# Performance work log

Measured on AMD Instinct MI355X. Metric: run time of the kernel, lower is better.

The kernel has to match this reference:

```python
import jax, jax.numpy as jnp
import numpy as np

D_MODEL = 1024
NUM_HEADS = 16
D_HEAD = D_MODEL // NUM_HEADS


def setup_inputs() -> dict:
    key = jax.random.key(0)
    kx, kq, kk, kv, ko = jax.random.split(key, 5)
    b, seq = 4, 2048
    x = jax.random.normal(kx, (b, seq, D_MODEL), dtype=jnp.float32)
    # Original uses ones for q/k/v and randn for output; use small random weights
    # for a numerically meaningful baseline of the same math.
    Wq = jax.random.normal(kq, (D_MODEL, D_MODEL), dtype=jnp.float32) * 0.02
    Wk = jax.random.normal(kk, (D_MODEL, D_MODEL), dtype=jnp.float32) * 0.02
    Wv = jax.random.normal(kv, (D_MODEL, D_MODEL), dtype=jnp.float32) * 0.02
    Wo = jax.random.normal(ko, (D_MODEL, D_MODEL), dtype=jnp.float32) * 0.02
    return {"x": x, "Wq": Wq, "Wk": Wk, "Wv": Wv, "Wo": Wo}


def reference(x, Wq, Wk, Wv, Wo):
    b, seq, d = x.shape
    h, dh = NUM_HEADS, D_HEAD

    def split_heads(t):  # [b, s, d] -> [b, h, s, dh]
        return t.reshape(b, seq, h, dh).transpose(0, 2, 1, 3)

    q = split_heads(x @ Wq.T)
    k = split_heads(x @ Wk.T)
    v = split_heads(x @ Wv.T)

    scores = jnp.einsum('bhqd,bhkd->bhqk', q, k) / jnp.sqrt(jnp.float32(dh))
    causal = jnp.tril(jnp.ones((seq, seq), dtype=bool))
    scores = jnp.where(causal, scores, -jnp.inf)
    attn = jax.nn.softmax(scores, axis=-1)
    out = jnp.einsum('bhqk,bhkd->bhqd', attn, v)  # [b, h, s, dh]
    out = out.transpose(0, 2, 1, 3).reshape(b, seq, d)
    return out @ Wo.T
```

## Files before the change

kernel.cpp:

```cpp
#include <hip/hip_runtime.h>
#include <stdint.h>

typedef unsigned short u16;
typedef __attribute__((ext_vector_type(8))) __bf16 bf16x8;
typedef __attribute__((ext_vector_type(4))) float f32x4;

#define AS1 __attribute__((address_space(1)))
#define AS3 __attribute__((address_space(3)))
#define LOG2E 1.4426950408889634f

#define BAR() __builtin_amdgcn_s_barrier()
#define VMC5() asm volatile("s_waitcnt vmcnt(5)" ::: "memory")
#define VMC0() asm volatile("s_waitcnt vmcnt(0)" ::: "memory")

__device__ __forceinline__ u16 f2bf(float f) {
    union { __bf16 h; u16 u; } cv;
    cv.h = (__bf16)f;
    return cv.u;
}

__device__ __forceinline__ float vmax4(f32x4 x) {
    return fmaxf(fmaxf(x[0], x[1]), fmaxf(x[2], x[3]));
}
__device__ __forceinline__ float vsum4(f32x4 x) {
    return (x[0] + x[1]) + (x[2] + x[3]);
}

__global__ __launch_bounds__(256) void cvt_kernel(
    const float* __restrict__ src, u16* __restrict__ dst, int n8)
{
    int i = blockIdx.x * 256 + threadIdx.x;
    if (i >= n8) return;
    const float4* s = (const float4*)src;
    float4 f0 = s[(size_t)i * 2], f1 = s[(size_t)i * 2 + 1];
    ushort4 a, b;
    a.x = f2bf(f0.x); a.y = f2bf(f0.y); a.z = f2bf(f0.z); a.w = f2bf(f0.w);
    b.x = f2bf(f1.x); b.y = f2bf(f1.y); b.z = f2bf(f1.z); b.w = f2bf(f1.w);
    ((ushort4*)dst)[(size_t)i * 2]     = a;
    ((ushort4*)dst)[(size_t)i * 2 + 1] = b;
}

__global__ __launch_bounds__(256) void cvt3_kernel(
    const float* __restrict__ wq, const float* __restrict__ wk,
    const float* __restrict__ wv, u16* __restrict__ dst)
{
    int i = blockIdx.x * 256 + threadIdx.x;
    int seg = i >> 17;
    const float* s = (seg == 0) ? wq : (seg == 1) ? wk : wv;
    float sc = (seg == 0) ? 0.125f : 1.0f;
    int j = i & 131071;
    const float4* sp = (const float4*)s;
    float4 f0 = sp[(size_t)j * 2], f1 = sp[(size_t)j * 2 + 1];
    ushort4 a, b;
    a.x = f2bf(f0.x * sc); a.y = f2bf(f0.y * sc); a.z = f2bf(f0.z * sc); a.w = f2bf(f0.w * sc);
    b.x = f2bf(f1.x * sc); b.y = f2bf(f1.y * sc); b.z = f2bf(f1.z * sc); b.w = f2bf(f1.w * sc);
    ((ushort4*)dst)[(size_t)i * 2]     = a;
    ((ushort4*)dst)[(size_t)i * 2 + 1] = b;
}

#define QBUF 28672

__device__ __forceinline__ void stage_A(
    const u16* __restrict__ G, int kt, int hm, u16* region, int t)
{
    int w6 = t & ~63;
#pragma unroll
    for (int i = 0; i < 2; ++i) {
        int s = i * 512 + t;
        int r = s >> 3;
        int j = (s & 7) ^ (r & 7);
        int row = (r & 63) + ((r >> 6) << 7) + (hm << 6);
        const u16* g = G + (size_t)row * 1024 + kt * 64 + j * 8;
        u16* lp = region + (i * 512 + w6) * 8;
        __builtin_amdgcn_global_load_lds((AS1 unsigned int*)g, (AS3 unsigned int*)lp, 16, 0, 0);
    }
}

__device__ __forceinline__ void stage_B01(
    const u16* __restrict__ G, int kt, u16* region, int t)
{
    int w6 = t & ~63;
#pragma unroll
    for (int i = 0; i < 2; ++i) {
        int s = i * 512 + t;
        int r = s >> 3;
        int j = (s & 7) ^ (r & 7);
        const u16* g = G + (size_t)r * 1024 + kt * 64 + j * 8;
        u16* lp = region + (i * 512 + w6) * 8;
        __builtin_amdgcn_global_load_lds((AS1 unsigned int*)g, (AS3 unsigned int*)lp, 16, 0, 0);
    }
}

__device__ __forceinline__ void stage_B2(
    const u16* __restrict__ G, int kt, u16* region, int t)
{
    int r = t >> 3;
    int j = (t & 7) ^ (r & 7);
    const u16* g = G + (size_t)(128 + r) * 1024 + kt * 64 + j * 8;
    u16* lp = region + 8192 + ((t & ~63)) * 8;
    __builtin_amdgcn_global_load_lds((AS1 unsigned int*)g, (AS3 unsigned int*)lp, 16, 0, 0);
}

__device__ __forceinline__ bf16x8 fragr(const u16* region, int row, int j) {
    int byte = row * 128 + ((j ^ (row & 7)) << 4);
    return *(const bf16x8*)((const char*)region + byte);
}

__global__ __launch_bounds__(512, 2) void gemm_qkv_256(
    const u16* __restrict__ X, const u16* __restrict__ W3, u16* __restrict__ QKV)
{
    __shared__ __attribute__((aligned(16))) u16 lds[57344];

    const int t  = threadIdx.x;
    const int l  = t & 63, w = t >> 6;
    const int wm = w >> 2, wn = w & 3;
    const int lr = l & 15, lg = l >> 4;

    int bid = (int)blockIdx.x;
    int wg  = (bid & 7) * 64 + (bid >> 3);
    int mx  = wg >> 4, ny = wg & 15;
    const int mb = mx * 256, nb = ny * 192;
    const u16* A = X  + (size_t)mb * 1024;
    const u16* B = W3 + (size_t)nb * 1024;

    const int NT = 16;

    stage_A  (A, 0, 0, lds + 0,             t);
    stage_B01(B, 0,    lds + 16384,         t);
    stage_B2 (B, 0,    lds + 16384,         t);
    stage_A  (A, 0, 1, lds + 8192,          t);
    stage_A  (A, 1, 0, lds + QBUF + 0,      t);
    stage_B01(B, 1,    lds + QBUF + 16384,  t);
    stage_B2 (B, 1,    lds + QBUF + 16384,  t);
    VMC5();
    BAR();

    f32x4 acc[8][3];
#pragma unroll
    for (int i = 0; i < 8; ++i)
#pragma unroll
        for (int j = 0; j < 3; ++j) acc[i][j] = f32x4{0.f, 0.f, 0.f, 0.f};

    const int brow0 = wn * 48;

    for (int kt = 0; kt < NT; ++kt) {
        const int p = kt & 1;
        u16* A0r = lds + p * QBUF;
        u16* A1r = A0r + 8192;
        u16* Br  = A0r + 16384;
        u16* A1n = lds + (p ^ 1) * QBUF + 8192;
        u16* Bn  = lds + p * QBUF + 16384;

        bf16x8 af[4][2], bf[3][2];

#pragma unroll
        for (int mi = 0; mi < 4; ++mi)
#pragma unroll
            for (int ks = 0; ks < 2; ++ks)
                af[mi][ks] = fragr(A0r, wm * 64 + mi * 16 + lr, ks * 4 + lg);
#pragma unroll
        for (int ni = 0; ni < 2; ++ni)
#pragma unroll
            for (int ks = 0; ks < 2; ++ks)
                bf[ni][ks] = fragr(Br, brow0 + ni * 16 + lr, ks * 4 + lg);
        if (kt + 1 < NT) stage_A(A, kt + 1, 1, A1n, t);
        BAR();
        __builtin_amdgcn_s_setprio(1);
#pragma unroll
        for (int mi = 0; mi < 4; ++mi)
#pragma unroll
            for (int ni = 0; ni < 2; ++ni)
#pragma unroll
                for (int ks = 0; ks < 2; ++ks)
                    acc[mi][ni] = __builtin_amdgcn_mfma_f32_16x16x32_bf16(af[mi][ks], bf[ni][ks], acc[mi][ni], 0, 0, 0);
        __builtin_amdgcn_s_setprio(0);
        BAR();

#pragma unroll
        for (int ks = 0; ks < 2; ++ks)
            bf[2][ks] = fragr(Br, brow0 + 32 + lr, ks * 4 + lg);
        if (kt + 2 < NT) stage_A(A, kt + 2, 0, A0r, t);
        BAR();
        __builtin_amdgcn_s_setprio(1);
#pragma unroll
        for (int mi = 0; mi < 4; ++mi)
#pragma unroll
            for (int ks = 0; ks < 2; ++ks)
                acc[mi][2] = __builtin_amdgcn_mfma_f32_16x16x32_bf16(af[mi][ks], bf[2][ks], acc[mi][2], 0, 0, 0);
        __builtin_amdgcn_s_setprio(0);
        BAR();

#pragma unroll
        for (int mi = 0; mi < 4; ++mi)
#pragma unroll
            for (int ks = 0; ks < 2; ++ks)
                af[mi][ks] = fragr(A1r, wm * 64 + mi * 16 + lr, ks * 4 + lg);
        if (kt + 2 < NT) stage_B01(B, kt + 2, Bn, t);
        BAR();
        __builtin_amdgcn_s_setprio(1);
#pragma unroll
        for (int mi = 0; mi < 4; ++mi)
#pragma unroll
            for (int ni = 0; ni < 2; ++ni)
#pragma unroll
                for (int ks = 0; ks < 2; ++ks)
                    acc[4 + mi][ni] = __builtin_amdgcn_mfma_f32_16x16x32_bf16(af[mi][ks], bf[ni][ks], acc[4 + mi][ni], 0, 0, 0);
        __builtin_amdgcn_s_setprio(0);
        BAR();

        if (kt + 2 < NT) {
            stage_B2(B, kt + 2, Bn, t);
            VMC5();
        } else if (kt + 1 < NT) {
            VMC0();
        }
        BAR();
        __builtin_amdgcn_s_setprio(1);
#pragma unroll
        for (int mi = 0; mi < 4; ++mi)
#pragma unroll
            for (int ks = 0; ks < 2; ++ks)
                acc[4 + mi][2] = __builtin_amdgcn_mfma_f32_16x16x32_bf16(af[mi][ks], bf[2][ks], acc[4 + mi][2], 0, 0, 0);
        __builtin_amdgcn_s_setprio(0);
        BAR();
    }

    u16* ep = lds;
#pragma unroll
    for (int mi = 0; mi < 8; ++mi) {
#pragma unroll
        for (int ni = 0; ni < 3; ++ni)
#pragma unroll
            for (int v = 0; v < 4; ++v)
                ep[(wm * 16 + lg * 4 + v) * 200 + wn * 48 + ni * 16 + lr] = f2bf(acc[mi][ni][v]);
        BAR();
#pragma unroll
        for (int c = 0; c < 2; ++c) {
            int ch = c * 512 + t;
            if (ch < 768) {
                int srow = ch / 24, col8 = (ch % 24) * 8;
                int grow = mb + (srow >> 4) * 128 + mi * 16 + (srow & 15);
                *(uint4*)(QKV + (size_t)grow * 3072 + nb + col8) =
                    *(const uint4*)(ep + srow * 200 + col8);
            }
        }
        BAR();
    }
}

__device__ __forceinline__ void gemm_tile_body_f32(
    const u16* __restrict__ A, const u16* __restrict__ B, float* __restrict__ Cp,
    int K, int ldc, int mb, int nb, u16* sh)
{
    u16* As = sh;
    u16* Bs = sh + 128 * 32;

    const int t  = threadIdx.x;
    const int l  = t & 63, w = t >> 6;
    const int wm = w >> 1, wn = w & 1;
    const int lr = l & 15, lg = l >> 4;

    f32x4 acc[4][4];
#pragma unroll
    for (int i = 0; i < 4; ++i)
#pragma unroll
        for (int j = 0; j < 4; ++j) acc[i][j] = f32x4{0.f, 0.f, 0.f, 0.f};

    for (int k0 = 0; k0 < K; k0 += 32) {
        __syncthreads();
#pragma unroll
        for (int i = 0; i < 2; ++i) {
            int chunk = i * 256 + t;
            int row   = chunk >> 2;
            int c8    = (chunk & 3) << 3;
            const u16* ga = A + (size_t)(mb + row) * K + k0 + c8;
            const u16* gb = B + (size_t)(nb + row) * K + k0 + c8;
            u16* la = As + (i * 256 + w * 64) * 8;
            u16* lb = Bs + (i * 256 + w * 64) * 8;
            __builtin_amdgcn_global_load_lds((AS1 unsigned int*)ga, (AS3 unsigned int*)la, 16, 0, 0);
            __builtin_amdgcn_global_load_lds((AS1 unsigned int*)gb, (AS3 unsigned int*)lb, 16, 0, 0);
        }
        __syncthreads();
        bf16x8 af[4], bfr[4];
#pragma unroll
        for (int mi = 0; mi < 4; ++mi)
            af[mi] = *(const bf16x8*)(As + (wm * 64 + mi * 16 + lr) * 32 + lg * 8);
#pragma unroll
        for (int ni = 0; ni < 4; ++ni)
            bfr[ni] = *(const bf16x8*)(Bs + (wn * 64 + ni * 16 + lr) * 32 + lg * 8);
#pragma unroll
        for (int mi = 0; mi < 4; ++mi)
#pragma unroll
            for (int ni = 0; ni < 4; ++ni)
                acc[mi][ni] = __builtin_amdgcn_mfma_f32_16x16x32_bf16(af[mi], bfr[ni], acc[mi][ni], 0, 0, 0);
    }

    __syncthreads();
    float* epf = (float*)sh;
#pragma unroll
    for (int s = 0; s < 8; ++s) {
        int wmS = s >> 2, miS = s & 3;
        if (wm == wmS) {
#pragma unroll
            for (int ni = 0; ni < 4; ++ni)
#pragma unroll
                for (int v = 0; v < 4; ++v)
                    epf[(lg * 4 + v) * 132 + wn * 64 + ni * 16 + lr] = acc[miS][ni][v];
        }
        __syncthreads();
#pragma unroll
        for (int c = 0; c < 2; ++c) {
            int ch = c * 256 + t;
            int srow = ch >> 5, c4 = (ch & 31) << 2;
            *(float4*)(Cp + (size_t)(mb + wmS * 64 + miS * 16 + srow) * ldc + nb + c4) =
                *(const float4*)(epf + srow * 132 + c4);
        }
        __syncthreads();
    }
}

__global__ __launch_bounds__(256, 2) void gemm_out_kernel(
    const u16* __restrict__ A, const u16* __restrict__ B, float* __restrict__ C)
{
    __shared__ __attribute__((aligned(16))) u16 sh[128 * 32 * 2];
    int bid = (int)blockIdx.x + (int)gridDim.x * (int)blockIdx.y;
    int wg  = (bid & 7) * 64 + (bid >> 3);
    int mx  = wg >> 3;
    int my  = wg & 7;
    gemm_tile_body_f32(A, B, C, 1024, 1024, mx * 128, my * 128, sh);
}

#define SEQ  2048
#define PSTR 72
#define NQT  16

__device__ __forceinline__ void attn_qtile(
    const u16* __restrict__ Qg, const u16* __restrict__ Kg, const u16* __restrict__ Vg,
    u16* __restrict__ outp, int b, int h, int qt,
    u16* QP, u16* Ks, u16* Vt)
{
    const int t  = threadIdx.x;
    const int l  = t & 63, w = t >> 6;
    const int lr = l & 15, lg = l >> 4;
    const int q0 = qt * 128;
    const int sr = t >> 3;
    const int sc = (t & 7) << 3;
    const int vswz = sc;

    __syncthreads();
#pragma unroll
    for (int i = 0; i < 4; ++i) {
        int r = sr + i * 32;
        *(uint4*)(QP + r * PSTR + sc) = *(const uint4*)(Qg + (size_t)(q0 + r) * 3072 + sc);
    }
    __syncthreads();
    bf16x8 qf[2][2];
#pragma unroll
    for (int mi = 0; mi < 2; ++mi)
#pragma unroll
        for (int ks = 0; ks < 2; ++ks)
            qf[mi][ks] = *(const bf16x8*)(QP + (w * 32 + mi * 16 + lr) * PSTR + ks * 32 + lg * 8);

    uint4 kpf[2], vpf[2];
#pragma unroll
    for (int i = 0; i < 2; ++i) {
        int r = sr + i * 32;
        kpf[i] = *(const uint4*)(Kg + (size_t)r * 3072 + sc);
        vpf[i] = *(const uint4*)(Vg + (size_t)r * 3072 + sc);
    }

    f32x4 o[4][2];
#pragma unroll
    for (int nd = 0; nd < 4; ++nd)
#pragma unroll
        for (int mi = 0; mi < 2; ++mi) o[nd][mi] = f32x4{0.f, 0.f, 0.f, 0.f};
    float mrow[2]  = { -__builtin_inff(), -__builtin_inff() };
    float mrowL[2] = { -__builtin_inff(), -__builtin_inff() };
    float lrow[2]  = { 0.f, 0.f };

    const int nkt = 2 * qt + 2;
    for (int kt = 0; kt < nkt; ++kt) {
        const int k0 = kt * 64;
        __syncthreads();
#pragma unroll
        for (int i = 0; i < 2; ++i) {
            int r = sr + i * 32;
            *(uint4*)(Ks + r * PSTR + sc) = kpf[i];
            int rs = r ^ vswz;
            union { uint4 q; u16 u[8]; } uv; uv.q = vpf[i];
#pragma unroll
            for (int j = 0; j < 8; ++j)
                Vt[(sc + j) * PSTR + rs] = uv.u[j];
        }
        if (kt + 1 < nkt) {
            const int k0n = k0 + 64;
#pragma unroll
            for (int i = 0; i < 2; ++i) {
                int r = sr + i * 32;
                kpf[i] = *(const uint4*)(Kg + (size_t)(k0n + r) * 3072 + sc);
                vpf[i] = *(const uint4*)(Vg + (size_t)(k0n + r) * 3072 + sc);
            }
        }
        __syncthreads();

        f32x4 s[4][2];
#pragma unroll
        for (int ni = 0; ni < 4; ++ni)
#pragma unroll
            for (int mi = 0; mi < 2; ++mi) s[ni][mi] = f32x4{0.f, 0.f, 0.f, 0.f};
        __builtin_amdgcn_s_setprio(1);
#pragma unroll
        for (int ks = 0; ks < 2; ++ks) {
            bf16x8 kb[4];
#pragma unroll
            for (int ni = 0; ni < 4; ++ni)
                kb[ni] = *(const bf16x8*)(Ks + (ni * 16 + lr) * PSTR + ks * 32 + lg * 8);
#pragma unroll
            for (int ni = 0; ni < 4; ++ni)
#pragma unroll
                for (int mi = 0; mi < 2; ++mi)
                    s[ni][mi] = __builtin_amdgcn_mfma_f32_16x16x32_bf16(kb[ni], qf[mi][ks], s[ni][mi], 0, 0, 0);
        }
        __builtin_amdgcn_s_setprio(0);

#pragma unroll
        for (int mi = 0; mi < 2; ++mi) {
            if ((k0 + 63) > (q0 + w * 32 + mi * 16)) {
                int qpos = q0 + w * 32 + mi * 16 + lr;
#pragma unroll
                for (int ni = 0; ni < 4; ++ni) {
                    int kb0 = k0 + ni * 16 + lg * 4;
#pragma unroll
                    for (int v = 0; v < 4; ++v)
                        if (kb0 + v > qpos) s[ni][mi][v] = -__builtin_inff();
                }
            }
        }

        float rmax[2];
        bool grew = false;
#pragma unroll
        for (int mi = 0; mi < 2; ++mi) {
            float r = fmaxf(fmaxf(vmax4(s[0][mi]), vmax4(s[1][mi])),
                            fmaxf(vmax4(s[2][mi]), vmax4(s[3][mi])));
            r = fmaxf(r, __shfl_xor(r, 16));
            r = fmaxf(r, __shfl_xor(r, 32));
            rmax[mi] = r;
            grew |= (r > mrow[mi]);
        }
        if (__ballot(grew)) {
#pragma unroll
            for (int mi = 0; mi < 2; ++mi) {
                float mn  = fmaxf(mrow[mi], rmax[mi]);
                float mnL = mn * LOG2E;
                float al  = __builtin_amdgcn_exp2f(mrowL[mi] - mnL);
                mrow[mi]  = mn;
                mrowL[mi] = mnL;
                lrow[mi] *= al;
#pragma unroll
                for (int nd = 0; nd < 4; ++nd)
#pragma unroll
                    for (int v = 0; v < 4; ++v) o[nd][mi][v] *= al;
            }
        }
#pragma unroll
        for (int mi = 0; mi < 2; ++mi) {
            float nmL = -mrowL[mi];
#pragma unroll
            for (int ni = 0; ni < 4; ++ni)
#pragma unroll
                for (int v = 0; v < 4; ++v)
                    s[ni][mi][v] = __builtin_amdgcn_exp2f(
                        __builtin_fmaf(s[ni][mi][v], LOG2E, nmL));
            float sum = (vsum4(s[0][mi]) + vsum4(s[1][mi]))
                      + (vsum4(s[2][mi]) + vsum4(s[3][mi]));
            sum += __shfl_xor(sum, 16);
            sum += __shfl_xor(sum, 32);
            lrow[mi] += sum;
            int prow = (w * 32 + mi * 16 + lr) * PSTR + lg * 4;
#pragma unroll
            for (int ni = 0; ni < 4; ++ni) {
                ushort4 u;
                u.x = f2bf(s[ni][mi][0]); u.y = f2bf(s[ni][mi][1]);
                u.z = f2bf(s[ni][mi][2]); u.w = f2bf(s[ni][mi][3]);
                *(ushort4*)(QP + prow + ni * 16) = u;
            }
        }

        __builtin_amdgcn_s_setprio(1);
#pragma unroll
        for (int ks = 0; ks < 2; ++ks) {
            bf16x8 pa[2], vb[4];
#pragma unroll
            for (int mi = 0; mi < 2; ++mi)
                pa[mi] = *(const bf16x8*)(QP + (w * 32 + mi * 16 + lr) * PSTR + ks * 32 + lg * 8);
#pragma unroll
            for (int nd = 0; nd < 4; ++nd) {
                int d = nd * 16 + lr;
                vb[nd] = *(const bf16x8*)(Vt + d * PSTR + ((ks * 32 + lg * 8) ^ (((d >> 3) & 7) << 3)));
            }
#pragma unroll
            for (int nd = 0; nd < 4; ++nd)
#pragma unroll
                for (int mi = 0; mi < 2; ++mi)
                    o[nd][mi] = __builtin_amdgcn_mfma_f32_16x16x32_bf16(vb[nd], pa[mi], o[nd][mi], 0, 0, 0);
        }
        __builtin_amdgcn_s_setprio(0);
    }

#pragma unroll
    for (int mi = 0; mi < 2; ++mi) {
        float inv = 1.f / lrow[mi];
        int row = q0 + w * 32 + mi * 16 + lr;
        u16* op = outp + (size_t)(b * SEQ + row) * 1024 + h * 64 + lg * 4;
#pragma unroll
        for (int nd = 0; nd < 4; ++nd) {
            ushort4 u;
            u.x = f2bf(o[nd][mi][0] * inv); u.y = f2bf(o[nd][mi][1] * inv);
            u.z = f2bf(o[nd][mi][2] * inv); u.w = f2bf(o[nd][mi][3] * inv);
            *(ushort4*)(op + nd * 16) = u;
        }
    }
}

__global__ __launch_bounds__(256, 2) void attn_kernel(
    const u16* __restrict__ qkv, u16* __restrict__ outp)
{
    __shared__ __attribute__((aligned(16))) u16 QP[128 * PSTR];
    __shared__ __attribute__((aligned(16))) u16 Ks[64 * PSTR];
    __shared__ __attribute__((aligned(16))) u16 Vt[64 * PSTR];

    const int bid = (int)blockIdx.x + (int)blockIdx.y * 8;
    const int xcd = bid & 7;
    const int j   = bid >> 3;
    const int bh  = xcd * 8 + (j & 7);
    const int qp  = j >> 3;
    const int b   = bh >> 4, h = bh & 15;

    const u16* Qg = qkv + (size_t)b * SEQ * 3072 + h * 64;
    const u16* Kg = Qg + 1024;
    const u16* Vg = Qg + 2048;

    attn_qtile(Qg, Kg, Vg, outp, b, h, qp,           QP, Ks, Vt);
    attn_qtile(Qg, Kg, Vg, outp, b, h, NQT - 1 - qp, QP, Ks, Vt);
}

extern "C" void kernel_launch(void* const* d_in, const int* in_sizes, int n_in,
                              void* d_out, int out_size, void* d_ws, size_t ws_size,
                              hipStream_t stream)
{
    (void)in_sizes; (void)n_in; (void)out_size; (void)ws_size;
    const float* x  = (const float*)d_in[0];
    const float* Wq = (const float*)d_in[1];
    const float* Wk = (const float*)d_in[2];
    const float* Wv = (const float*)d_in[3];
    const float* Wo = (const float*)d_in[4];

    u16*   qkv = (u16*)d_ws;
    u16*   xb  = qkv + (size_t)8192 * 3072;
    u16*   att = xb;
    u16*   w3  = (u16*)d_out;
    u16*   wob = qkv;
    float* out = (float*)d_out;

    cvt_kernel <<<dim3(4096), 256, 0, stream>>>(x, xb, 1048576);
    cvt3_kernel<<<dim3(1536), 256, 0, stream>>>(Wq, Wk, Wv, w3);

    gemm_qkv_256<<<dim3(512), 512, 0, stream>>>(xb, w3, qkv);
    attn_kernel <<<dim3(8, 64), 256, 0, stream>>>(qkv, att);

    cvt_kernel<<<dim3(512), 256, 0, stream>>>(Wo, wob, 131072);
    gemm_out_kernel<<<dim3(64, 8), 256, 0, stream>>>(att, wob, out);
}
```

Before: 272.5 us.

## Use two-phase double-buffered pipelines for both GEMMs and fuse input conversions

Merges the x and Wq/Wk/Wv bf16 conversion kernels into one launch. The QKV GEMM's four-phase interleaved staging with partial vmcnt waits is replaced by a simpler prefetch-next-tile double buffer with one barrier per K step. The output GEMM is rewritten with K=64 swizzled LDS tiles and double buffering instead of single-buffered K=32 loads. This targets load latency and barrier overhead in the output GEMM, but the simpler QKV schedule may expose more memory latency.

```diff
diff --git a/kernel.cpp b/kernel.cpp
--- a/kernel.cpp
+++ b/kernel.cpp
@@ -8,10 +8,6 @@
 #define AS1 __attribute__((address_space(1)))
 #define AS3 __attribute__((address_space(3)))
 #define LOG2E 1.4426950408889634f
-
-#define BAR() __builtin_amdgcn_s_barrier()
-#define VMC5() asm volatile("s_waitcnt vmcnt(5)" ::: "memory")
-#define VMC0() asm volatile("s_waitcnt vmcnt(0)" ::: "memory")
 
 __device__ __forceinline__ u16 f2bf(float f) {
     union { __bf16 h; u16 u; } cv;
@@ -24,6 +20,32 @@
 }
 __device__ __forceinline__ float vsum4(f32x4 x) {
     return (x[0] + x[1]) + (x[2] + x[3]);
+}
+
+__global__ __launch_bounds__(256) void cvt_all(
+    const float* __restrict__ x,  const float* __restrict__ wq,
+    const float* __restrict__ wk, const float* __restrict__ wv,
+    u16* __restrict__ xb, u16* __restrict__ w3)
+{
+    int i = blockIdx.x * 256 + threadIdx.x;
+    const float* s; u16* d; float sc = 1.0f; int j;
+    if (i < 1048576) {
+        s = x; d = xb; j = i;
+    } else {
+        int k = i - 1048576;
+        int seg = k >> 17;
+        j = k & 131071;
+        s = (seg == 0) ? wq : (seg == 1) ? wk : wv;
+        sc = (seg == 0) ? 0.125f : 1.0f;
+        d = w3 + ((size_t)seg << 20);
+    }
+    const float4* sp = (const float4*)s;
+    float4 f0 = sp[(size_t)j * 2], f1 = sp[(size_t)j * 2 + 1];
+    ushort4 a, b;
+    a.x = f2bf(f0.x * sc); a.y = f2bf(f0.y * sc); a.z = f2bf(f0.z * sc); a.w = f2bf(f0.w * sc);
+    b.x = f2bf(f1.x * sc); b.y = f2bf(f1.y * sc); b.z = f2bf(f1.z * sc); b.w = f2bf(f1.w * sc);
+    ((ushort4*)d)[(size_t)j * 2]     = a;
+    ((ushort4*)d)[(size_t)j * 2 + 1] = b;
 }
 
 __global__ __launch_bounds__(256) void cvt_kernel(
@@ -40,24 +62,6 @@
     ((ushort4*)dst)[(size_t)i * 2 + 1] = b;
 }
 
-__global__ __launch_bounds__(256) void cvt3_kernel(
-    const float* __restrict__ wq, const float* __restrict__ wk,
-    const float* __restrict__ wv, u16* __restrict__ dst)
-{
-    int i = blockIdx.x * 256 + threadIdx.x;
-    int seg = i >> 17;
-    const float* s = (seg == 0) ? wq : (seg == 1) ? wk : wv;
-    float sc = (seg == 0) ? 0.125f : 1.0f;
-    int j = i & 131071;
-    const float4* sp = (const float4*)s;
-    float4 f0 = sp[(size_t)j * 2], f1 = sp[(size_t)j * 2 + 1];
-    ushort4 a, b;
-    a.x = f2bf(f0.x * sc); a.y = f2bf(f0.y * sc); a.z = f2bf(f0.z * sc); a.w = f2bf(f0.w * sc);
-    b.x = f2bf(f1.x * sc); b.y = f2bf(f1.y * sc); b.z = f2bf(f1.z * sc); b.w = f2bf(f1.w * sc);
-    ((ushort4*)dst)[(size_t)i * 2]     = a;
-    ((ushort4*)dst)[(size_t)i * 2 + 1] = b;
-}
-
 #define QBUF 28672
 
 __device__ __forceinline__ void stage_A(
@@ -106,7 +110,7 @@
     return *(const bf16x8*)((const char*)region + byte);
 }
 
-__global__ __launch_bounds__(512, 2) void gemm_qkv_256(
+__global__ __launch_bounds__(512, 2) void gemm_qkv_2ph(
     const u16* __restrict__ X, const u16* __restrict__ W3, u16* __restrict__ QKV)
 {
     __shared__ __attribute__((aligned(16))) u16 lds[57344];
@@ -125,15 +129,11 @@
 
     const int NT = 16;
 
-    stage_A  (A, 0, 0, lds + 0,             t);
-    stage_B01(B, 0,    lds + 16384,         t);
-    stage_B2 (B, 0,    lds + 16384,         t);
-    stage_A  (A, 0, 1, lds + 8192,          t);
-    stage_A  (A, 1, 0, lds + QBUF + 0,      t);
-    stage_B01(B, 1,    lds + QBUF + 16384,  t);
-    stage_B2 (B, 1,    lds + QBUF + 16384,  t);
-    VMC5();
-    BAR();
+    stage_A  (A, 0, 0, lds + 0,     t);
+    stage_A  (A, 0, 1, lds + 8192,  t);
+    stage_B01(B, 0,    lds + 16384, t);
+    stage_B2 (B, 0,    lds + 16384, t);
+    __syncthreads();
 
     f32x4 acc[8][3];
 #pragma unroll
@@ -145,84 +145,52 @@
 
     for (int kt = 0; kt < NT; ++kt) {
         const int p = kt & 1;
-        u16* A0r = lds + p * QBUF;
-        u16* A1r = A0r + 8192;
-        u16* Br  = A0r + 16384;
-        u16* A1n = lds + (p ^ 1) * QBUF + 8192;
-        u16* Bn  = lds + p * QBUF + 16384;
-
-        bf16x8 af[4][2], bf[3][2];
-
+        u16* cur = lds + p * QBUF;
+        u16* nxt = lds + (p ^ 1) * QBUF;
+
+        if (kt + 1 < NT) {
+            stage_A  (A, kt + 1, 0, nxt,         t);
+            stage_A  (A, kt + 1, 1, nxt + 8192,  t);
+            stage_B01(B, kt + 1,    nxt + 16384, t);
+            stage_B2 (B, kt + 1,    nxt + 16384, t);
+        }
+
+        bf16x8 bf[3][2], af[4][2];
+#pragma unroll
+        for (int ni = 0; ni < 3; ++ni)
+#pragma unroll
+            for (int ks = 0; ks < 2; ++ks)
+                bf[ni][ks] = fragr(cur + 16384, brow0 + ni * 16 + lr, ks * 4 + lg);
 #pragma unroll
         for (int mi = 0; mi < 4; ++mi)
 #pragma unroll
             for (int ks = 0; ks < 2; ++ks)
-                af[mi][ks] = fragr(A0r, wm * 64 + mi * 16 + lr, ks * 4 + lg);
-#pragma unroll
-        for (int ni = 0; ni < 2; ++ni)
-#pragma unroll
-            for (int ks = 0; ks < 2; ++ks)
-                bf[ni][ks] = fragr(Br, brow0 + ni * 16 + lr, ks * 4 + lg);
-        if (kt + 1 < NT) stage_A(A, kt + 1, 1, A1n, t);
-        BAR();
+                af[mi][ks] = fragr(cur, wm * 64 + mi * 16 + lr, ks * 4 + lg);
         __builtin_amdgcn_s_setprio(1);
 #pragma unroll
         for (int mi = 0; mi < 4; ++mi)
 #pragma unroll
-            for (int ni = 0; ni < 2; ++ni)
+            for (int ni = 0; ni < 3; ++ni)
 #pragma unroll
                 for (int ks = 0; ks < 2; ++ks)
                     acc[mi][ni] = __builtin_amdgcn_mfma_f32_16x16x32_bf16(af[mi][ks], bf[ni][ks], acc[mi][ni], 0, 0, 0);
         __builtin_amdgcn_s_setprio(0);
-        BAR();
-
-#pragma unroll
-        for (int ks = 0; ks < 2; ++ks)
-            bf[2][ks] = fragr(Br, brow0 + 32 + lr, ks * 4 + lg);
-        if (kt + 2 < NT) stage_A(A, kt + 2, 0, A0r, t);
-        BAR();
+#pragma unroll
+        for (int mi = 0; mi < 4; ++mi)
+#pragma unroll
+            for (int ks = 0; ks < 2; ++ks)
+                af[mi][ks] = fragr(cur + 8192, wm * 64 + mi * 16 + lr, ks * 4 + lg);
         __builtin_amdgcn_s_setprio(1);
 #pragma unroll
         for (int mi = 0; mi < 4; ++mi)
 #pragma unroll
-            for (int ks = 0; ks < 2; ++ks)
-                acc[mi][2] = __builtin_amdgcn_mfma_f32_16x16x32_bf16(af[mi][ks], bf[2][ks], acc[mi][2], 0, 0, 0);
-        __builtin_amdgcn_s_setprio(0);
-        BAR();
-
-#pragma unroll
-        for (int mi = 0; mi < 4; ++mi)
-#pragma unroll
-            for (int ks = 0; ks < 2; ++ks)
-                af[mi][ks] = fragr(A1r, wm * 64 + mi * 16 + lr, ks * 4 + lg);
-        if (kt + 2 < NT) stage_B01(B, kt + 2, Bn, t);
-        BAR();
-        __builtin_amdgcn_s_setprio(1);
-#pragma unroll
-        for (int mi = 0; mi < 4; ++mi)
-#pragma unroll
-            for (int ni = 0; ni < 2; ++ni)
+            for (int ni = 0; ni < 3; ++ni)
 #pragma unroll
                 for (int ks = 0; ks < 2; ++ks)
                     acc[4 + mi][ni] = __builtin_amdgcn_mfma_f32_16x16x32_bf16(af[mi][ks], bf[ni][ks], acc[4 + mi][ni], 0, 0, 0);
         __builtin_amdgcn_s_setprio(0);
-        BAR();
-
-        if (kt + 2 < NT) {
-            stage_B2(B, kt + 2, Bn, t);
-            VMC5();
-        } else if (kt + 1 < NT) {
-            VMC0();
-        }
-        BAR();
-        __builtin_amdgcn_s_setprio(1);
-#pragma unroll
-        for (int mi = 0; mi < 4; ++mi)
-#pragma unroll
-            for (int ks = 0; ks < 2; ++ks)
-                acc[4 + mi][2] = __builtin_amdgcn_mfma_f32_16x16x32_bf16(af[mi][ks], bf[2][ks], acc[4 + mi][2], 0, 0, 0);
-        __builtin_amdgcn_s_setprio(0);
-        BAR();
+
+        __syncthreads();
     }
 
     u16* ep = lds;
@@ -233,7 +201,7 @@
 #pragma unroll
             for (int v = 0; v < 4; ++v)
                 ep[(wm * 16 + lg * 4 + v) * 200 + wn * 48 + ni * 16 + lr] = f2bf(acc[mi][ni][v]);
-        BAR();
+        __syncthreads();
 #pragma unroll
         for (int c = 0; c < 2; ++c) {
             int ch = c * 512 + t;
@@ -244,59 +212,89 @@
                     *(const uint4*)(ep + srow * 200 + col8);
             }
         }
-        BAR();
-    }
-}
-
-__device__ __forceinline__ void gemm_tile_body_f32(
-    const u16* __restrict__ A, const u16* __restrict__ B, float* __restrict__ Cp,
-    int K, int ldc, int mb, int nb, u16* sh)
-{
-    u16* As = sh;
-    u16* Bs = sh + 128 * 32;
+        __syncthreads();
+    }
+}
+
+__device__ __forceinline__ void stage_128(
+    const u16* __restrict__ G, int kt, u16* region, int t)
+{
+    int w6 = t & ~63;
+#pragma unroll
+    for (int i = 0; i < 4; ++i) {
+        int s = i * 256 + t;
+        int r = s >> 3;
+        int j = (s & 7) ^ (r & 7);
+        const u16* g = G + (size_t)r * 1024 + kt * 64 + j * 8;
+        u16* lp = region + (i * 256 + w6) * 8;
+        __builtin_amdgcn_global_load_lds((AS1 unsigned int*)g, (AS3 unsigned int*)lp, 16, 0, 0);
+    }
+}
+
+__global__ __launch_bounds__(256, 2) void gemm_out_2ph(
+    const u16* __restrict__ Ag, const u16* __restrict__ Bg, float* __restrict__ C)
+{
+    __shared__ __attribute__((aligned(16))) u16 lds[32768];
 
     const int t  = threadIdx.x;
     const int l  = t & 63, w = t >> 6;
     const int wm = w >> 1, wn = w & 1;
     const int lr = l & 15, lg = l >> 4;
 
+    int bid = (int)blockIdx.x;
+    int wg  = (bid & 7) * 64 + (bid >> 3);
+    int mx  = wg >> 3, my = wg & 7;
+    const int mb = mx * 128, nb = my * 128;
+    const u16* A = Ag + (size_t)mb * 1024;
+    const u16* B = Bg + (size_t)nb * 1024;
+
+    const int NT = 16;
+
+    stage_128(A, 0, lds + 0,    t);
+    stage_128(B, 0, lds + 8192, t);
+    __syncthreads();
+
     f32x4 acc[4][4];
 #pragma unroll
     for (int i = 0; i < 4; ++i)
 #pragma unroll
         for (int j = 0; j < 4; ++j) acc[i][j] = f32x4{0.f, 0.f, 0.f, 0.f};
 
-    for (int k0 = 0; k0 < K; k0 += 32) {
-        __syncthreads();
-#pragma unroll
-        for (int i = 0; i < 2; ++i) {
-            int chunk = i * 256 + t;
-            int row   = chunk >> 2;
-            int c8    = (chunk & 3) << 3;
-            const u16* ga = A + (size_t)(mb + row) * K + k0 + c8;
-            const u16* gb = B + (size_t)(nb + row) * K + k0 + c8;
-            u16* la = As + (i * 256 + w * 64) * 8;
-            u16* lb = Bs + (i * 256 + w * 64) * 8;
-            __builtin_amdgcn_global_load_lds((AS1 unsigned int*)ga, (AS3 unsigned int*)la, 16, 0, 0);
-            __builtin_amdgcn_global_load_lds((AS1 unsigned int*)gb, (AS3 unsigned int*)lb, 16, 0, 0);
-        }
-        __syncthreads();
-        bf16x8 af[4], bfr[4];
+    for (int kt = 0; kt < NT; ++kt) {
+        const int p = kt & 1;
+        u16* cur = lds + p * 16384;
+        u16* nxt = lds + (p ^ 1) * 16384;
+
+        if (kt + 1 < NT) {
+            stage_128(A, kt + 1, nxt,        t);
+            stage_128(B, kt + 1, nxt + 8192, t);
+        }
+
+        bf16x8 af[4][2], bf[4][2];
 #pragma unroll
         for (int mi = 0; mi < 4; ++mi)
-            af[mi] = *(const bf16x8*)(As + (wm * 64 + mi * 16 + lr) * 32 + lg * 8);
+#pragma unroll
+            for (int ks = 0; ks < 2; ++ks)
+                af[mi][ks] = fragr(cur, wm * 64 + mi * 16 + lr, ks * 4 + lg);
 #pragma unroll
         for (int ni = 0; ni < 4; ++ni)
-            bfr[ni] = *(const bf16x8*)(Bs + (wn * 64 + ni * 16 + lr) * 32 + lg * 8);
+#pragma unroll
+            for (int ks = 0; ks < 2; ++ks)
+                bf[ni][ks] = fragr(cur + 8192, wn * 64 + ni * 16 + lr, ks * 4 + lg);
+        __builtin_amdgcn_s_setprio(1);
 #pragma unroll
         for (int mi = 0; mi < 4; ++mi)
 #pragma unroll
             for (int ni = 0; ni < 4; ++ni)
-                acc[mi][ni] = __builtin_amdgcn_mfma_f32_16x16x32_bf16(af[mi], bfr[ni], acc[mi][ni], 0, 0, 0);
-    }
-
-    __syncthreads();
-    float* epf = (float*)sh;
+#pragma unroll
+                for (int ks = 0; ks < 2; ++ks)
+                    acc[mi][ni] = __builtin_amdgcn_mfma_f32_16x16x32_bf16(af[mi][ks], bf[ni][ks], acc[mi][ni], 0, 0, 0);
+        __builtin_amdgcn_s_setprio(0);
+
+        __syncthreads();
+    }
+
+    float* epf = (float*)lds;
 #pragma unroll
     for (int s = 0; s < 8; ++s) {
         int wmS = s >> 2, miS = s & 3;
@@ -312,22 +310,11 @@
         for (int c = 0; c < 2; ++c) {
             int ch = c * 256 + t;
             int srow = ch >> 5, c4 = (ch & 31) << 2;
-            *(float4*)(Cp + (size_t)(mb + wmS * 64 + miS * 16 + srow) * ldc + nb + c4) =
+            *(float4*)(C + (size_t)(mb + wmS * 64 + miS * 16 + srow) * 1024 + nb + c4) =
                 *(const float4*)(epf + srow * 132 + c4);
         }
         __syncthreads();
     }
-}
-
-__global__ __launch_bounds__(256, 2) void gemm_out_kernel(
-    const u16* __restrict__ A, const u16* __restrict__ B, float* __restrict__ C)
-{
-    __shared__ __attribute__((aligned(16))) u16 sh[128 * 32 * 2];
-    int bid = (int)blockIdx.x + (int)gridDim.x * (int)blockIdx.y;
-    int wg  = (bid & 7) * 64 + (bid >> 3);
-    int mx  = wg >> 3;
-    int my  = wg & 7;
-    gemm_tile_body_f32(A, B, C, 1024, 1024, mx * 128, my * 128, sh);
 }
 
 #define SEQ  2048
@@ -563,12 +550,11 @@
     u16*   wob = qkv;
     float* out = (float*)d_out;
 
-    cvt_kernel <<<dim3(4096), 256, 0, stream>>>(x, xb, 1048576);
-    cvt3_kernel<<<dim3(1536), 256, 0, stream>>>(Wq, Wk, Wv, w3);
-
-    gemm_qkv_256<<<dim3(512), 512, 0, stream>>>(xb, w3, qkv);
+    cvt_all<<<dim3(5632), 256, 0, stream>>>(x, Wq, Wk, Wv, xb, w3);
+
+    gemm_qkv_2ph<<<dim3(512), 512, 0, stream>>>(xb, w3, qkv);
     attn_kernel <<<dim3(8, 64), 256, 0, stream>>>(qkv, att);
 
     cvt_kernel<<<dim3(512), 256, 0, stream>>>(Wo, wob, 131072);
-    gemm_out_kernel<<<dim3(64, 8), 256, 0, stream>>>(att, wob, out);
-}
+    gemm_out_2ph<<<dim3(512), 256, 0, stream>>>(att, wob, out);
+}
```

Result: faster. 249.7 us (-8.4%).
